# Kernel tuning notes

Measured on AMD Instinct MI355X. Metric: run time of the kernel, lower is better.

The kernel has to match this reference:

```python
import jax, jax.numpy as jnp
import numpy as np

B, S, D = 4, 2048, 1024
H = 3 * D  # MLP hidden


def setup_inputs() -> dict:
    key = jax.random.key(0)
    ks = jax.random.split(key, 12)
    s = 1.0 / np.sqrt(D)
    n = lambda k, shape, sc: (jax.random.normal(k, shape, jnp.float32) * sc)
    return {
        "x": n(ks[0], (B, S, D), 1.0),
        "ln1_g": jnp.ones((D,), jnp.float32), "ln1_b": jnp.zeros((D,), jnp.float32),
        "ln2_g": jnp.ones((D,), jnp.float32), "ln2_b": jnp.zeros((D,), jnp.float32),
        "Wq": n(ks[1], (D, D), s), "bq": jnp.zeros((D,), jnp.float32),
        "Wk": n(ks[2], (D, D), s), "bk": jnp.zeros((D,), jnp.float32),
        "Wv": n(ks[3], (D, D), s), "bv": jnp.zeros((D,), jnp.float32),
        "Wi": n(ks[4], (D, 1), s), "bi": jnp.zeros((1,), jnp.float32),
        "Wf": n(ks[5], (D, 1), s), "bf": jnp.zeros((1,), jnp.float32),
        "Wo": n(ks[6], (D, D), s), "bo": jnp.zeros((D,), jnp.float32),
        "W1": n(ks[7], (D, H), s), "b1": jnp.zeros((H,), jnp.float32),
        "W2": n(ks[8], (H, D), 1.0 / np.sqrt(H)), "b2": jnp.zeros((D,), jnp.float32),
    }


def _layernorm(x, g, b, eps=1e-5):
    m = jnp.mean(x, axis=-1, keepdims=True)
    v = jnp.mean(jnp.square(x - m), axis=-1, keepdims=True)
    return (x - m) * jax.lax.rsqrt(v + eps) * g + b


def reference(x, ln1_g, ln1_b, ln2_g, ln2_b, Wq, bq, Wk, bk, Wv, bv,
              Wi, bi, Wf, bf, Wo, bo, W1, b1, W2, b2):
    seq = x.shape[1]
    h = _layernorm(x, ln1_g, ln1_b)
    # q, k computed in the original but unused in the score matrix (kept faithful)
    q = h @ Wq + bq
    k = h @ Wk + bk
    v = h @ Wv + bv                                  # [B,S,D]
    log_f = jax.nn.log_sigmoid(h @ Wf + bf)          # [B,S,1]
    log_i = jax.nn.log_sigmoid(h @ Wi + bi)          # [B,S,1]
    o = jax.nn.sigmoid(h @ Wo + bo)                  # [B,S,D]
    log_f_cum = jnp.cumsum(log_f, axis=1)            # [B,S,1]
    # log_scores[b,t,s] = log_i[b,s] + log_f_cum[b,t] - log_f_cum[b,s]
    log_scores = jnp.swapaxes(log_i, 1, 2) + log_f_cum - jnp.swapaxes(log_f_cum, 1, 2)
    causal = jnp.triu(jnp.full((seq, seq), -1e9, jnp.float32), k=1)
    scores = jnp.exp(log_scores + causal[None])      # [B,S,S]
    scores = scores / (jnp.sum(scores, axis=-1, keepdims=True) + 1e-6)
    attn = scores @ v                                # [B,S,D]
    x = x + o * attn
    h2 = _layernorm(x, ln2_g, ln2_b)
    m = h2 @ W1 + b1
    m = jnp.square(jnp.where(m > 0, m, 0.01 * m))    # LeakyReLU then square
    x = x + m @ W2 + b2
    return x
```

## Files before the change

kernel.cpp:

```cpp
#include <hip/hip_runtime.h>
#include <hip/hip_bf16.h>
#include <cstdint>

#define DI __device__ __forceinline__
typedef unsigned short u16;
using f32x4 = __attribute__((ext_vector_type(4))) float;
using bf16x8 = __attribute__((ext_vector_type(8))) short;

DI float bf16_bits_to_f32(u16 h) { return __uint_as_float(((unsigned int)h) << 16); }
DI u16 f32_to_bf16_bits(float f) {
    unsigned int u = __float_as_uint(f);
    unsigned int lsb = (u >> 16) & 1u;
    u += 0x7fffu + lsb;
    return (u16)(u >> 16);
}
DI float logsigf(float z) {
    if (z >= 0.f) return -log1pf(expf(-z));
    return z - log1pf(expf(z));
}
DI float lsef(float a, float b) {
    float mx = fmaxf(a, b), mn = fminf(a, b);
    return mx + log1pf(expf(mn - mx));
}
DI void ld4(float* d, const float* s) { *(float4*)d = *(const float4*)s; }

struct __align__(8) U4 { u16 a, b, c, d; };
union BF8 { u16 s[8]; uint4 v; };

DI void gload_lds16(const void* gsrc, void* ldst) {
    __builtin_amdgcn_global_load_lds(
        (const __attribute__((address_space(1))) uint32_t*)gsrc,
        (__attribute__((address_space(3))) uint32_t*)ldst,
        16, 0, 0);
}

__global__ void detect_kernel(const unsigned int* __restrict__ g1, int* __restrict__ flag) {
    if (threadIdx.x == 0 && blockIdx.x == 0)
        flag[0] = (g1[0] == 0x3F803F80u) ? 1 : 0;
}

struct SmallConv {
    const void* src[12];
    unsigned int dstOff[12];
    int n[12];
};
__global__ __launch_bounds__(256) void conv_small(
    SmallConv sc, float* __restrict__ wsf, const int* __restrict__ flag)
{
    const bool isbf = (flag[0] != 0);
    const int e = blockIdx.x;
    const void* s = sc.src[e];
    float* d = wsf + sc.dstOff[e];
    const int n = sc.n[e];
    for (int i = threadIdx.x; i < n; i += 256)
        d[i] = isbf ? bf16_bits_to_f32(((const u16*)s)[i]) : ((const float*)s)[i];
}

struct TransDesc {
    const void* src[4];
    unsigned int dstOff[4];
    int R[4], Cd[4];
    int start[5];
};
__global__ __launch_bounds__(256) void transpose_all(
    TransDesc td, u16* __restrict__ wsb, const int* __restrict__ flag)
{
    __shared__ float tile[64][65];
    const bool isbf = (flag[0] != 0);
    const int bid = blockIdx.x;
    int e = 0;
    if (bid >= td.start[1]) e = 1;
    if (bid >= td.start[2]) e = 2;
    if (bid >= td.start[3]) e = 3;
    const int local = bid - td.start[e];
    const int R = td.R[e], Cd = td.Cd[e];
    const int nbx = R >> 6;
    const int r0 = (local % nbx) * 64, c0 = (local / nbx) * 64;
    const void* src = td.src[e];
    u16* dst = wsb + td.dstOff[e];
    const int tid = threadIdx.x;
    #pragma unroll
    for (int i = 0; i < 16; ++i) {
        int idx = tid + i * 256;
        int lr = idx >> 6, lc = idx & 63;
        size_t g = (size_t)(r0 + lr) * Cd + c0 + lc;
        tile[lr][lc] = isbf ? bf16_bits_to_f32(((const u16*)src)[g]) : ((const float*)src)[g];
    }
    __syncthreads();
    #pragma unroll
    for (int i = 0; i < 16; ++i) {
        int idx = tid + i * 256;
        int lc2 = idx >> 6, lr2 = idx & 63;
        dst[(size_t)(c0 + lc2) * R + r0 + lr2] = f32_to_bf16_bits(tile[lr2][lc2]);
    }
}

DI float block_reduce_sum256(float v, float* sbuf) {
    #pragma unroll
    for (int off = 32; off > 0; off >>= 1) v += __shfl_down(v, off);
    int lane = threadIdx.x & 63, wid = threadIdx.x >> 6;
    if (lane == 0) sbuf[wid] = v;
    __syncthreads();
    float r = sbuf[0] + sbuf[1] + sbuf[2] + sbuf[3];
    __syncthreads();
    return r;
}

template<bool FI, bool RAW>
__global__ __launch_bounds__(256) void ln_kernel(
    const void* __restrict__ Xv, const int* __restrict__ flag,
    const float* __restrict__ gam, const float* __restrict__ bet,
    u16* __restrict__ Hout,
    const float* __restrict__ Wi, const float* __restrict__ bi,
    const float* __restrict__ Wf, const float* __restrict__ bf2,
    float* __restrict__ li, float* __restrict__ lf)
{
    __shared__ float sbuf[4];
    int row = blockIdx.x;
    int tid = threadIdx.x;
    size_t base = (size_t)row * 1024 + (size_t)tid * 4;
    float x[4];
    if (RAW && flag[0] != 0) {
        U4 u = *(const U4*)((const u16*)Xv + base);
        x[0] = bf16_bits_to_f32(u.a); x[1] = bf16_bits_to_f32(u.b);
        x[2] = bf16_bits_to_f32(u.c); x[3] = bf16_bits_to_f32(u.d);
    } else {
        ld4(x, (const float*)Xv + base);
    }
    float s = x[0] + x[1] + x[2] + x[3];
    s = block_reduce_sum256(s, sbuf);
    float mean = s * (1.f / 1024.f);
    float d[4], ss = 0.f;
    #pragma unroll
    for (int j = 0; j < 4; ++j) { d[j] = x[j] - mean; ss += d[j] * d[j]; }
    ss = block_reduce_sum256(ss, sbuf);
    float rstd = rsqrtf(ss * (1.f / 1024.f) + 1e-5f);
    float g4[4], b4[4];
    ld4(g4, gam + tid * 4); ld4(b4, bet + tid * 4);
    float h[4];
    #pragma unroll
    for (int j = 0; j < 4; ++j) h[j] = d[j] * rstd * g4[j] + b4[j];
    U4 hu;
    hu.a = f32_to_bf16_bits(h[0]); hu.b = f32_to_bf16_bits(h[1]);
    hu.c = f32_to_bf16_bits(h[2]); hu.d = f32_to_bf16_bits(h[3]);
    *(U4*)(Hout + base) = hu;
    if (FI) {
        float wi4[4], wf4[4];
        ld4(wi4, Wi + tid * 4); ld4(wf4, Wf + tid * 4);
        float pi = 0.f, pf = 0.f;
        #pragma unroll
        for (int j = 0; j < 4; ++j) { pi += h[j] * wi4[j]; pf += h[j] * wf4[j]; }
        pi = block_reduce_sum256(pi, sbuf);
        pf = block_reduce_sum256(pf, sbuf);
        if (tid == 0) {
            li[row] = logsigf(pi + bi[0]);
            lf[row] = logsigf(pf + bf2[0]);
        }
    }
}

__global__ __launch_bounds__(1024) void gates_kernel(
    const float* __restrict__ lf, const float* __restrict__ li,
    float* __restrict__ F, float* __restrict__ rsinv, int S)
{
    __shared__ float p[1024];
    __shared__ float q[1024];
    int b = blockIdx.x, t = threadIdx.x;
    float a = lf[b * S + 2 * t], c = lf[b * S + 2 * t + 1];
    float s2 = a + c;
    p[t] = s2; __syncthreads();
    #pragma unroll
    for (int off = 1; off < 1024; off <<= 1) {
        float add = (t >= off) ? p[t - off] : 0.f;
        __syncthreads();
        p[t] += add;
        __syncthreads();
    }
    float excl = p[t] - s2;
    float F0 = excl + a, F1 = excl + s2;
    F[b * S + 2 * t] = F0; F[b * S + 2 * t + 1] = F1;
    float g0 = li[b * S + 2 * t] - F0;
    float g1 = li[b * S + 2 * t + 1] - F1;
    float m2 = lsef(g0, g1);
    q[t] = m2; __syncthreads();
    #pragma unroll
    for (int off = 1; off < 1024; off <<= 1) {
        float add = (t >= off) ? q[t - off] : -1e30f;
        __syncthreads();
        float nv = lsef(q[t], add);
        __syncthreads();
        q[t] = nv;
        __syncthreads();
    }
    float lprev = (t > 0) ? q[t - 1] : -1e30f;
    float lc0 = lsef(lprev, g0);
    float lc1 = q[t];
    rsinv[b * S + 2 * t]     = 1.f / (expf(F0 + lc0) + 1e-6f);
    rsinv[b * S + 2 * t + 1] = 1.f / (expf(F1 + lc1) + 1e-6f);
}

__global__ __launch_bounds__(256) void wgen_kernel(
    const float* __restrict__ li, const float* __restrict__ F,
    const float* __restrict__ rsinv, u16* __restrict__ Wn)
{
    const int S = 2048;
    const int st = blockIdx.x, i = blockIdx.y, b = blockIdx.z;
    if (st >= 2 * i + 2) return;
    const int t0 = i * 128, s0 = st * 64;
    const int tid = threadIdx.x;
    const int lane = tid & 63, wave = tid >> 6;
    const int colb = (lane & 7) * 8;
    float lv[8], fv[8];
    ld4(lv, li + b * S + s0 + colb); ld4(lv + 4, li + b * S + s0 + colb + 4);
    ld4(fv, F + b * S + s0 + colb);  ld4(fv + 4, F + b * S + s0 + colb + 4);
    float g[8];
    #pragma unroll
    for (int j = 0; j < 8; ++j) g[j] = lv[j] - fv[j];
    #pragma unroll
    for (int r = 0; r < 4; ++r) {
        int row = wave * 32 + r * 8 + (lane >> 3);
        int t = t0 + row;
        float Ft = F[b * S + t];
        float ri = rsinv[b * S + t];
        BF8 wb;
        #pragma unroll
        for (int j = 0; j < 8; ++j) {
            int sg = s0 + colb + j;
            float w = (sg <= t) ? expf(g[j] + Ft) * ri : 0.f;
            wb.s[j] = f32_to_bf16_bits(w);
        }
        *(uint4*)(Wn + ((size_t)b * S + t) * S + s0 + colb) = wb.v;
    }
}

template<int EPI>
__global__ __launch_bounds__(256) void gemm_bt(
    const u16* __restrict__ A, const u16* __restrict__ Bt,
    const float* __restrict__ bias, u16* __restrict__ C,
    const float* __restrict__ resid, void* __restrict__ outp,
    const int* __restrict__ flag, int M, int N, int K)
{
    __shared__ short As[128 * 64];
    __shared__ short Bs[128 * 64];
    const int tid = threadIdx.x;
    const int lane = tid & 63;
    const int wave = tid >> 6;
    const int wm = wave >> 1, wn = wave & 1;
    const int m0 = blockIdx.x * 128, n0 = blockIdx.y * 128;

    const int srow = tid >> 3;
    const int sk = ((tid & 7) ^ (srow & 7)) * 8;
    const u16* aB = A  + (size_t)(m0 + srow) * K + sk;
    const u16* bB = Bt + (size_t)(n0 + srow) * K + sk;
    const size_t rowK32 = (size_t)32 * K;
    char* AsB = (char*)As + wave * 1024;
    char* BsB = (char*)Bs + wave * 1024;

    const int hi = lane >> 4;
    const int l7 = lane & 7;
    int ar[4], br[4];
    #pragma unroll
    for (int f = 0; f < 4; ++f) {
        ar[f] = (wm * 64 + f * 16 + (lane & 15)) * 64;
        br[f] = (wn * 64 + f * 16 + (lane & 15)) * 64;
    }

    f32x4 acc[4][4] = {};

    for (int k0 = 0; k0 < K; k0 += 64) {
        const u16* ga = aB; const u16* gb = bB;
        #pragma unroll
        for (int p = 0; p < 4; ++p) { gload_lds16(ga, AsB + p * 4096); ga += rowK32; }
        #pragma unroll
        for (int p = 0; p < 4; ++p) { gload_lds16(gb, BsB + p * 4096); gb += rowK32; }
        aB += 64; bB += 64;
        __syncthreads();
        #pragma unroll
        for (int kk = 0; kk < 2; ++kk) {
            const int co = ((kk * 4 + hi) ^ l7) * 8;
            bf16x8 af[4], bv[4];
            #pragma unroll
            for (int f = 0; f < 4; ++f) af[f] = *(const bf16x8*)&As[ar[f] + co];
            #pragma unroll
            for (int f = 0; f < 4; ++f) bv[f] = *(const bf16x8*)&Bs[br[f] + co];
            #pragma unroll
            for (int mf = 0; mf < 4; ++mf)
                #pragma unroll
                for (int nf = 0; nf < 4; ++nf)
                    acc[mf][nf] = __builtin_amdgcn_mfma_f32_16x16x32_bf16(
                        af[mf], bv[nf], acc[mf][nf], 0, 0, 0);
        }
        __syncthreads();
    }

    const bool outbf = (EPI == 3) ? (flag[0] != 0) : false;
    #pragma unroll
    for (int mf = 0; mf < 4; ++mf) {
        int r0 = m0 + wm * 64 + mf * 16 + (lane >> 4) * 4;
        #pragma unroll
        for (int nf = 0; nf < 4; ++nf) {
            int col = n0 + wn * 64 + nf * 16 + (lane & 15);
            float bsc = (EPI == 4) ? 0.f : bias[col];
            #pragma unroll
            for (int j = 0; j < 4; ++j) {
                int row = r0 + j;
                float v = acc[mf][nf][j] + ((EPI == 4) ? bias[row] : bsc);
                if constexpr (EPI == 4) {
                    C[(size_t)row * N + col] = f32_to_bf16_bits(v);
                } else if constexpr (EPI == 1) {
                    C[(size_t)row * N + col] = f32_to_bf16_bits(1.f / (1.f + expf(-v)));
                } else if constexpr (EPI == 2) {
                    float l = v > 0.f ? v : 0.01f * v;
                    C[(size_t)row * N + col] = f32_to_bf16_bits(l * l);
                } else {
                    size_t gi = (size_t)row * N + col;
                    v += resid[gi];
                    if (outbf) ((u16*)outp)[gi] = f32_to_bf16_bits(v);
                    else       ((float*)outp)[gi] = v;
                }
            }
        }
    }
}

__global__ __launch_bounds__(256) void attn_gemm(
    const u16* __restrict__ Wn, const u16* __restrict__ Vt,
    const u16* __restrict__ Ob, const void* __restrict__ Xraw,
    const int* __restrict__ flag, float* __restrict__ XF)
{
    const int S = 2048, D = 1024, NT = 8192;
    __shared__ short As[128 * 64];
    __shared__ short Bs[128 * 64];
    const int b  = blockIdx.z;
    const int it = 15 - blockIdx.x;
    const int t0 = it * 128;
    const int d0 = blockIdx.y * 128;
    const int tid = threadIdx.x;
    const int lane = tid & 63;
    const int wave = tid >> 6;
    const int wm = wave >> 1, wn = wave & 1;

    const int srow = tid >> 3;
    const int sk = ((tid & 7) ^ (srow & 7)) * 8;
    const u16* aB = Wn + ((size_t)b * S + t0 + srow) * S + sk;
    const u16* bB = Vt + (size_t)(d0 + srow) * NT + b * S + sk;
    char* AsB = (char*)As + wave * 1024;
    char* BsB = (char*)Bs + wave * 1024;

    const int hi = lane >> 4;
    const int l7 = lane & 7;
    int ar[4], br[4];
    #pragma unroll
    for (int f = 0; f < 4; ++f) {
        ar[f] = (wm * 64 + f * 16 + (lane & 15)) * 64;
        br[f] = (wn * 64 + f * 16 + (lane & 15)) * 64;
    }

    f32x4 acc[4][4] = {};
    const int nst = 2 * it + 2;
    for (int st = 0; st < nst; ++st) {
        const int s0 = st * 64;
        const u16* ga = aB + s0; const u16* gb = bB + s0;
        #pragma unroll
        for (int p = 0; p < 4; ++p) { gload_lds16(ga, AsB + p * 4096); ga += (size_t)32 * S; }
        #pragma unroll
        for (int p = 0; p < 4; ++p) { gload_lds16(gb, BsB + p * 4096); gb += (size_t)32 * NT; }
        __syncthreads();
        #pragma unroll
        for (int kk = 0; kk < 2; ++kk) {
            const int co = ((kk * 4 + hi) ^ l7) * 8;
            bf16x8 af[4], bv[4];
            #pragma unroll
            for (int f = 0; f < 4; ++f) af[f] = *(const bf16x8*)&As[ar[f] + co];
            #pragma unroll
            for (int f = 0; f < 4; ++f) bv[f] = *(const bf16x8*)&Bs[br[f] + co];
            #pragma unroll
            for (int mf = 0; mf < 4; ++mf)
                #pragma unroll
                for (int nf = 0; nf < 4; ++nf)
                    acc[mf][nf] = __builtin_amdgcn_mfma_f32_16x16x32_bf16(
                        af[mf], bv[nf], acc[mf][nf], 0, 0, 0);
        }
        __syncthreads();
    }

    const bool isbf = (flag[0] != 0);
    #pragma unroll
    for (int mf = 0; mf < 4; ++mf) {
        #pragma unroll
        for (int j = 0; j < 4; ++j) {
            int r = wm * 64 + mf * 16 + (lane >> 4) * 4 + j;
            int t = t0 + r;
            #pragma unroll
            for (int nf = 0; nf < 4; ++nf) {
                int dcol = d0 + wn * 64 + nf * 16 + (lane & 15);
                size_t base = ((size_t)b * S + t) * D + dcol;
                float o = bf16_bits_to_f32(Ob[base]);
                float xv = isbf ? bf16_bits_to_f32(((const u16*)Xraw)[base])
                                : ((const float*)Xraw)[base];
                XF[base] = xv + o * acc[mf][nf][j];
            }
        }
    }
}

static constexpr size_t OFB_LI   = 4096;
static constexpr size_t OFB_LF   = 36864;
static constexpr size_t OFB_F    = 69632;
static constexpr size_t OFB_G1   = 102400;
static constexpr size_t OFB_B1LN = 106496;
static constexpr size_t OFB_G2   = 110592;
static constexpr size_t OFB_B2LN = 114688;
static constexpr size_t OFB_BV   = 118784;
static constexpr size_t OFB_BO   = 122880;
static constexpr size_t OFB_WI   = 126976;
static constexpr size_t OFB_WF   = 131072;
static constexpr size_t OFB_B1   = 135168;
static constexpr size_t OFB_B2B  = 147456;
static constexpr size_t OFB_BI   = 151552;
static constexpr size_t OFB_BF   = 152576;
static constexpr size_t OFB_RS   = 200704;
static constexpr size_t OFB_XF   = 1048576;
static constexpr size_t OFB_H    = OFB_XF + 33554432;
static constexpr size_t OFB_V    = OFB_H + 16777216;
static constexpr size_t OFB_O    = OFB_V + 16777216;
static constexpr size_t OFB_M    = OFB_O + 16777216;
static constexpr size_t OFB_WVT  = OFB_M + 50331648;
static constexpr size_t OFB_WOT  = OFB_WVT + 2097152;
static constexpr size_t OFB_W1T  = OFB_WOT + 2097152;
static constexpr size_t OFB_W2T  = OFB_W1T + 6291456;
static constexpr size_t WS_BYTES = OFB_W2T + 6291456;

extern "C" void kernel_launch(void* const* d_in, const int* in_sizes, int n_in,
                              void* d_out, int out_size, void* d_ws, size_t ws_size,
                              hipStream_t stream) {
    (void)in_sizes; (void)n_in; (void)out_size;
    if (ws_size < WS_BYTES) return;
    char* ws = (char*)d_ws;
    int* flag = (int*)ws;
    auto FP = [&](size_t off) { return (float*)(ws + off); };
    auto HP = [&](size_t off) { return (u16*)(ws + off); };

    detect_kernel<<<1, 64, 0, stream>>>((const unsigned int*)d_in[1], flag);

    SmallConv sc;
    const int   srcIdx[12] = {1, 2, 3, 4, 10, 16, 11, 12, 13, 14, 18, 20};
    const size_t dstOff[12] = {OFB_G1, OFB_B1LN, OFB_G2, OFB_B2LN, OFB_BV, OFB_BO,
                               OFB_WI, OFB_BI, OFB_WF, OFB_BF, OFB_B1, OFB_B2B};
    const int   cnt[12] = {1024, 1024, 1024, 1024, 1024, 1024, 1024, 1, 1024, 1, 3072, 1024};
    for (int e = 0; e < 12; ++e) {
        sc.src[e] = d_in[srcIdx[e]];
        sc.dstOff[e] = (unsigned int)(dstOff[e] / 4);
        sc.n[e] = cnt[e];
    }
    conv_small<<<12, 256, 0, stream>>>(sc, (float*)ws, flag);

    TransDesc td;
    td.src[0] = d_in[9];  td.dstOff[0] = (unsigned int)(OFB_WVT / 2); td.R[0] = 1024; td.Cd[0] = 1024;
    td.src[1] = d_in[15]; td.dstOff[1] = (unsigned int)(OFB_WOT / 2); td.R[1] = 1024; td.Cd[1] = 1024;
    td.src[2] = d_in[17]; td.dstOff[2] = (unsigned int)(OFB_W1T / 2); td.R[2] = 1024; td.Cd[2] = 3072;
    td.src[3] = d_in[19]; td.dstOff[3] = (unsigned int)(OFB_W2T / 2); td.R[3] = 3072; td.Cd[3] = 1024;
    td.start[0] = 0; td.start[1] = 256; td.start[2] = 512; td.start[3] = 1280; td.start[4] = 2048;
    transpose_all<<<2048, 256, 0, stream>>>(td, (u16*)ws, flag);

    ln_kernel<true, true><<<8192, 256, 0, stream>>>(
        d_in[0], flag, FP(OFB_G1), FP(OFB_B1LN), HP(OFB_H),
        FP(OFB_WI), FP(OFB_BI), FP(OFB_WF), FP(OFB_BF),
        FP(OFB_LI), FP(OFB_LF));

    gates_kernel<<<4, 1024, 0, stream>>>(FP(OFB_LF), FP(OFB_LI), FP(OFB_F), FP(OFB_RS), 2048);

    wgen_kernel<<<dim3(32, 16, 4), 256, 0, stream>>>(
        FP(OFB_LI), FP(OFB_F), FP(OFB_RS), HP(OFB_M));

    gemm_bt<4><<<dim3(8, 64), 256, 0, stream>>>(
        HP(OFB_WVT), HP(OFB_H), FP(OFB_BV), HP(OFB_V),
        nullptr, nullptr, flag, 1024, 8192, 1024);
    gemm_bt<1><<<dim3(64, 8), 256, 0, stream>>>(
        HP(OFB_H), HP(OFB_WOT), FP(OFB_BO), HP(OFB_O),
        nullptr, nullptr, flag, 8192, 1024, 1024);

    attn_gemm<<<dim3(16, 8, 4), 256, 0, stream>>>(
        HP(OFB_M), HP(OFB_V), HP(OFB_O), d_in[0], flag, FP(OFB_XF));

    ln_kernel<false, false><<<8192, 256, 0, stream>>>(
        FP(OFB_XF), flag, FP(OFB_G2), FP(OFB_B2LN), HP(OFB_H),
        nullptr, nullptr, nullptr, nullptr, nullptr, nullptr);

    gemm_bt<2><<<dim3(64, 24), 256, 0, stream>>>(
        HP(OFB_H), HP(OFB_W1T), FP(OFB_B1), HP(OFB_M),
        nullptr, nullptr, flag, 8192, 3072, 1024);
    gemm_bt<3><<<dim3(64, 8), 256, 0, stream>>>(
        HP(OFB_M), HP(OFB_W2T), FP(OFB_B2B), nullptr,
        FP(OFB_XF), d_out, flag, 8192, 1024, 3072);
}
```

Baseline: 323.0 us.

## Switch GEMMs to 32x32x16 MFMA and shrink M tiles for more blocks

```diff
diff --git a/kernel.cpp b/kernel.cpp
--- a/kernel.cpp
+++ b/kernel.cpp
@@ -4,7 +4,7 @@
 
 #define DI __device__ __forceinline__
 typedef unsigned short u16;
-using f32x4 = __attribute__((ext_vector_type(4))) float;
+using f32x16 = __attribute__((ext_vector_type(16))) float;
 using bf16x8 = __attribute__((ext_vector_type(8))) short;
 
 DI float bf16_bits_to_f32(u16 h) { return __uint_as_float(((unsigned int)h) << 16); }
@@ -233,20 +233,21 @@
     }
 }
 
-template<int EPI>
-__global__ __launch_bounds__(256) void gemm_bt(
+template<int EPI, int TM>
+__global__ __launch_bounds__(256) void gemm32(
     const u16* __restrict__ A, const u16* __restrict__ Bt,
     const float* __restrict__ bias, u16* __restrict__ C,
     const float* __restrict__ resid, void* __restrict__ outp,
     const int* __restrict__ flag, int M, int N, int K)
 {
-    __shared__ short As[128 * 64];
+    constexpr int MF = TM / 64;
+    __shared__ short As[TM * 64];
     __shared__ short Bs[128 * 64];
     const int tid = threadIdx.x;
     const int lane = tid & 63;
     const int wave = tid >> 6;
     const int wm = wave >> 1, wn = wave & 1;
-    const int m0 = blockIdx.x * 128, n0 = blockIdx.y * 128;
+    const int m0 = blockIdx.x * TM, n0 = blockIdx.y * 128;
 
     const int srow = tid >> 3;
     const int sk = ((tid & 7) ^ (srow & 7)) * 8;
@@ -256,38 +257,36 @@
     char* AsB = (char*)As + wave * 1024;
     char* BsB = (char*)Bs + wave * 1024;
 
-    const int hi = lane >> 4;
-    const int l7 = lane & 7;
-    int ar[4], br[4];
-    #pragma unroll
-    for (int f = 0; f < 4; ++f) {
-        ar[f] = (wm * 64 + f * 16 + (lane & 15)) * 64;
-        br[f] = (wn * 64 + f * 16 + (lane & 15)) * 64;
-    }
-
-    f32x4 acc[4][4] = {};
+    const int l31 = lane & 31, hi2 = lane >> 5, l7 = lane & 7;
+    int ar[MF], br[2];
+    #pragma unroll
+    for (int f = 0; f < MF; ++f) ar[f] = (wm * (TM / 2) + f * 32 + l31) * 64;
+    #pragma unroll
+    for (int f = 0; f < 2; ++f)  br[f] = (wn * 64 + f * 32 + l31) * 64;
+
+    f32x16 acc[MF][2] = {};
 
     for (int k0 = 0; k0 < K; k0 += 64) {
         const u16* ga = aB; const u16* gb = bB;
         #pragma unroll
-        for (int p = 0; p < 4; ++p) { gload_lds16(ga, AsB + p * 4096); ga += rowK32; }
+        for (int p = 0; p < TM / 32; ++p) { gload_lds16(ga, AsB + p * 4096); ga += rowK32; }
         #pragma unroll
         for (int p = 0; p < 4; ++p) { gload_lds16(gb, BsB + p * 4096); gb += rowK32; }
         aB += 64; bB += 64;
         __syncthreads();
         #pragma unroll
-        for (int kk = 0; kk < 2; ++kk) {
-            const int co = ((kk * 4 + hi) ^ l7) * 8;
-            bf16x8 af[4], bv[4];
+        for (int kc = 0; kc < 4; ++kc) {
+            const int co = ((kc * 2 + hi2) ^ l7) * 8;
+            bf16x8 af[MF], bv[2];
             #pragma unroll
-            for (int f = 0; f < 4; ++f) af[f] = *(const bf16x8*)&As[ar[f] + co];
+            for (int f = 0; f < MF; ++f) af[f] = *(const bf16x8*)&As[ar[f] + co];
             #pragma unroll
-            for (int f = 0; f < 4; ++f) bv[f] = *(const bf16x8*)&Bs[br[f] + co];
+            for (int f = 0; f < 2; ++f)  bv[f] = *(const bf16x8*)&Bs[br[f] + co];
             #pragma unroll
-            for (int mf = 0; mf < 4; ++mf)
+            for (int mf = 0; mf < MF; ++mf)
                 #pragma unroll
-                for (int nf = 0; nf < 4; ++nf)
-                    acc[mf][nf] = __builtin_amdgcn_mfma_f32_16x16x32_bf16(
+                for (int nf = 0; nf < 2; ++nf)
+                    acc[mf][nf] = __builtin_amdgcn_mfma_f32_32x32x16_bf16(
                         af[mf], bv[nf], acc[mf][nf], 0, 0, 0);
         }
         __syncthreads();
@@ -295,16 +294,15 @@
 
     const bool outbf = (EPI == 3) ? (flag[0] != 0) : false;
     #pragma unroll
-    for (int mf = 0; mf < 4; ++mf) {
-        int r0 = m0 + wm * 64 + mf * 16 + (lane >> 4) * 4;
-        #pragma unroll
-        for (int nf = 0; nf < 4; ++nf) {
-            int col = n0 + wn * 64 + nf * 16 + (lane & 15);
+    for (int mf = 0; mf < MF; ++mf) {
+        #pragma unroll
+        for (int nf = 0; nf < 2; ++nf) {
+            int col = n0 + wn * 64 + nf * 32 + l31;
             float bsc = (EPI == 4) ? 0.f : bias[col];
             #pragma unroll
-            for (int j = 0; j < 4; ++j) {
-                int row = r0 + j;
-                float v = acc[mf][nf][j] + ((EPI == 4) ? bias[row] : bsc);
+            for (int reg = 0; reg < 16; ++reg) {
+                int row = m0 + wm * (TM / 2) + mf * 32 + hi2 * 4 + (reg & 3) + 8 * (reg >> 2);
+                float v = acc[mf][nf][reg] + ((EPI == 4) ? bias[row] : bsc);
                 if constexpr (EPI == 4) {
                     C[(size_t)row * N + col] = f32_to_bf16_bits(v);
                 } else if constexpr (EPI == 1) {
@@ -323,17 +321,17 @@
     }
 }
 
-__global__ __launch_bounds__(256) void attn_gemm(
+__global__ __launch_bounds__(256) void attn32(
     const u16* __restrict__ Wn, const u16* __restrict__ Vt,
     const u16* __restrict__ Ob, const void* __restrict__ Xraw,
     const int* __restrict__ flag, float* __restrict__ XF)
 {
     const int S = 2048, D = 1024, NT = 8192;
-    __shared__ short As[128 * 64];
+    __shared__ short As[64 * 64];
     __shared__ short Bs[128 * 64];
     const int b  = blockIdx.z;
-    const int it = 15 - blockIdx.x;
-    const int t0 = it * 128;
+    const int it = 31 - (int)blockIdx.x;
+    const int t0 = it * 64;
     const int d0 = blockIdx.y * 128;
     const int tid = threadIdx.x;
     const int lane = tid & 63;
@@ -347,59 +345,46 @@
     char* AsB = (char*)As + wave * 1024;
     char* BsB = (char*)Bs + wave * 1024;
 
-    const int hi = lane >> 4;
-    const int l7 = lane & 7;
-    int ar[4], br[4];
-    #pragma unroll
-    for (int f = 0; f < 4; ++f) {
-        ar[f] = (wm * 64 + f * 16 + (lane & 15)) * 64;
-        br[f] = (wn * 64 + f * 16 + (lane & 15)) * 64;
-    }
-
-    f32x4 acc[4][4] = {};
-    const int nst = 2 * it + 2;
+    const int l31 = lane & 31, hi2 = lane >> 5, l7 = lane & 7;
+    const int ar0 = (wm * 32 + l31) * 64;
+    int br[2];
+    #pragma unroll
+    for (int f = 0; f < 2; ++f) br[f] = (wn * 64 + f * 32 + l31) * 64;
+
+    f32x16 acc[2] = {};
+    const int nst = it + 1;
     for (int st = 0; st < nst; ++st) {
         const int s0 = st * 64;
         const u16* ga = aB + s0; const u16* gb = bB + s0;
         #pragma unroll
-        for (int p = 0; p < 4; ++p) { gload_lds16(ga, AsB + p * 4096); ga += (size_t)32 * S; }
+        for (int p = 0; p < 2; ++p) { gload_lds16(ga, AsB + p * 4096); ga += (size_t)32 * S; }
         #pragma unroll
         for (int p = 0; p < 4; ++p) { gload_lds16(gb, BsB + p * 4096); gb += (size_t)32 * NT; }
         __syncthreads();
         #pragma unroll
-        for (int kk = 0; kk < 2; ++kk) {
-            const int co = ((kk * 4 + hi) ^ l7) * 8;
-            bf16x8 af[4], bv[4];
-            #pragma unroll
-            for (int f = 0; f < 4; ++f) af[f] = *(const bf16x8*)&As[ar[f] + co];
-            #pragma unroll
-            for (int f = 0; f < 4; ++f) bv[f] = *(const bf16x8*)&Bs[br[f] + co];
-            #pragma unroll
-            for (int mf = 0; mf < 4; ++mf)
-                #pragma unroll
-                for (int nf = 0; nf < 4; ++nf)
-                    acc[mf][nf] = __builtin_amdgcn_mfma_f32_16x16x32_bf16(
-                        af[mf], bv[nf], acc[mf][nf], 0, 0, 0);
+        for (int kc = 0; kc < 4; ++kc) {
+            const int co = ((kc * 2 + hi2) ^ l7) * 8;
+            bf16x8 af = *(const bf16x8*)&As[ar0 + co];
+            bf16x8 bv0 = *(const bf16x8*)&Bs[br[0] + co];
+            bf16x8 bv1 = *(const bf16x8*)&Bs[br[1] + co];
+            acc[0] = __builtin_amdgcn_mfma_f32_32x32x16_bf16(af, bv0, acc[0], 0, 0, 0);
+            acc[1] = __builtin_amdgcn_mfma_f32_32x32x16_bf16(af, bv1, acc[1], 0, 0, 0);
         }
         __syncthreads();
     }
 
     const bool isbf = (flag[0] != 0);
     #pragma unroll
-    for (int mf = 0; mf < 4; ++mf) {
-        #pragma unroll
-        for (int j = 0; j < 4; ++j) {
-            int r = wm * 64 + mf * 16 + (lane >> 4) * 4 + j;
-            int t = t0 + r;
-            #pragma unroll
-            for (int nf = 0; nf < 4; ++nf) {
-                int dcol = d0 + wn * 64 + nf * 16 + (lane & 15);
-                size_t base = ((size_t)b * S + t) * D + dcol;
-                float o = bf16_bits_to_f32(Ob[base]);
-                float xv = isbf ? bf16_bits_to_f32(((const u16*)Xraw)[base])
-                                : ((const float*)Xraw)[base];
-                XF[base] = xv + o * acc[mf][nf][j];
-            }
+    for (int nf = 0; nf < 2; ++nf) {
+        int dcol = d0 + wn * 64 + nf * 32 + l31;
+        #pragma unroll
+        for (int reg = 0; reg < 16; ++reg) {
+            int t = t0 + wm * 32 + hi2 * 4 + (reg & 3) + 8 * (reg >> 2);
+            size_t base = ((size_t)b * S + t) * D + dcol;
+            float o = bf16_bits_to_f32(Ob[base]);
+            float xv = isbf ? bf16_bits_to_f32(((const u16*)Xraw)[base])
+                            : ((const float*)Xraw)[base];
+            XF[base] = xv + o * acc[nf][reg];
         }
     }
 }
@@ -473,24 +458,24 @@
     wgen_kernel<<<dim3(32, 16, 4), 256, 0, stream>>>(
         FP(OFB_LI), FP(OFB_F), FP(OFB_RS), HP(OFB_M));
 
-    gemm_bt<4><<<dim3(8, 64), 256, 0, stream>>>(
+    gemm32<4, 64><<<dim3(16, 64), 256, 0, stream>>>(
         HP(OFB_WVT), HP(OFB_H), FP(OFB_BV), HP(OFB_V),
         nullptr, nullptr, flag, 1024, 8192, 1024);
-    gemm_bt<1><<<dim3(64, 8), 256, 0, stream>>>(
+    gemm32<1, 64><<<dim3(128, 8), 256, 0, stream>>>(
         HP(OFB_H), HP(OFB_WOT), FP(OFB_BO), HP(OFB_O),
         nullptr, nullptr, flag, 8192, 1024, 1024);
 
-    attn_gemm<<<dim3(16, 8, 4), 256, 0, stream>>>(
+    attn32<<<dim3(32, 8, 4), 256, 0, stream>>>(
         HP(OFB_M), HP(OFB_V), HP(OFB_O), d_in[0], flag, FP(OFB_XF));
 
     ln_kernel<false, false><<<8192, 256, 0, stream>>>(
         FP(OFB_XF), flag, FP(OFB_G2), FP(OFB_B2LN), HP(OFB_H),
         nullptr, nullptr, nullptr, nullptr, nullptr, nullptr);
 
-    gemm_bt<2><<<dim3(64, 24), 256, 0, stream>>>(
+    gemm32<2, 128><<<dim3(64, 24), 256, 0, stream>>>(
         HP(OFB_H), HP(OFB_W1T), FP(OFB_B1), HP(OFB_M),
         nullptr, nullptr, flag, 8192, 3072, 1024);
-    gemm_bt<3><<<dim3(64, 8), 256, 0, stream>>>(
+    gemm32<3, 64><<<dim3(128, 8), 256, 0, stream>>>(
         HP(OFB_M), HP(OFB_W2T), FP(OFB_B2B), nullptr,
         FP(OFB_XF), d_out, flag, 8192, 1024, 3072);
 }
```

Measured after the change: 361.6 us. 1.12x slower.
